# Kernel tuning notes

Measured on AMD Instinct MI355X. Metric: run time of the kernel, lower is better.

## Reference

```python
import jax, jax.numpy as jnp
import numpy as np

B, N = 64, 1500
F_MIN, F_MAX = 0.5, 3.0  # HR band in Hz (30-180 bpm)
SAMPLING_F = 0.002       # frequency grid step -> F = 1251 frequencies
FS = 30.0                # video frame rate


def setup_inputs() -> dict:
    key = jax.random.key(0)
    k1, k2 = jax.random.split(key)
    x = jax.random.normal(k1, (B, N), dtype=jnp.float32)
    # true frequencies inside the searched band
    f_true = jax.random.uniform(k2, (B,), dtype=jnp.float32, minval=F_MIN, maxval=F_MAX)
    fs = jnp.full((B,), FS, dtype=jnp.float32)
    deltas = jnp.zeros((B,), dtype=jnp.float32)  # accepted but unused by the loss
    return {
        "x": x,
        "f_true": f_true,
        "fs": fs,
        "deltas": deltas,
        "sampling_f": SAMPLING_F,
        "f_range": (F_MIN, F_MAX),
    }


def reference(x, f_true, fs, deltas, sampling_f, f_range):
    f_min, f_max = f_range
    # frequency grid, same semantics as torch.arange(f_min, f_max+step, step)
    f_values = jnp.arange(f_min, f_max + sampling_f, sampling_f, dtype=jnp.float32)  # [F]
    n = jnp.arange(x.shape[1], dtype=jnp.float32)  # [N] time indices
    # angles[b,f,n] = 2*pi * f_values[f] * n / fs[b]  (fs varies per sample)
    phase = (2.0 * jnp.pi) * (f_values[None, :, None] * n[None, None, :]) / fs[:, None, None]  # [B,F,N]
    # PSD at each grid frequency: (sum x cos)^2 + (sum x sin)^2, batched as one contraction
    cos_terms = jnp.einsum('bn,bfn->bf', x, jnp.cos(phase))  # [B,F]
    sin_terms = jnp.einsum('bn,bfn->bf', x, jnp.sin(phase))  # [B,F]
    psd = cos_terms ** 2 + sin_terms ** 2                    # [B,F]
    log_lik = jnp.log(jax.nn.softmax(psd, axis=1) + 1e-8)    # [B,F]
    # index of grid frequency closest to f_true (non-differentiable gather index)
    idx = jnp.argmin(jnp.abs(f_values[None, :] - f_true[:, None]), axis=1)  # [B]
    per_sample = -jnp.take_along_axis(log_lik, idx[:, None], axis=1)[:, 0]  # [B]
    return jnp.mean(per_sample)
```

## Files before the change

kernel.cpp:

```cpp
#include <hip/hip_runtime.h>

#define BATCH 64
#define NSAMP 1500
#define NFREQ 1251
#define NSEG  5
#define SEGLEN 300
#define FBLK  256
#define FCHUNKS 5

__global__ __launch_bounds__(256) void goertzel_kernel(
    const float* __restrict__ x,
    const float* __restrict__ fs,
    const float* __restrict__ sampling_f,
    const float* __restrict__ f_range,
    float2* __restrict__ pcs,
    float* __restrict__ out)
{
    __shared__ float4 xs4[SEGLEN / 4];
    const int b   = blockIdx.x;
    const int seg = blockIdx.z;
    const int tid = threadIdx.x;
    const int n0  = seg * SEGLEN;

    if (b == 0 && seg == 0 && blockIdx.y == 0 && tid == 0) out[0] = 0.0f;

    const float4* xg = reinterpret_cast<const float4*>(x + b * NSAMP + n0);
    for (int i = tid; i < SEGLEN / 4; i += FBLK) xs4[i] = xg[i];
    __syncthreads();

    const int fidx = blockIdx.y * FBLK + tid;
    if (fidx >= NFREQ) return;

    const float f_min = f_range[0];
    const float step  = sampling_f[0];
    const float delta = (f_min + step) - f_min;
    const float fv    = f_min + (float)fidx * delta;

    const float rho = fv / fs[b];
    float rf = rho - floorf(rho);
    const float coef = 2.0f * __builtin_amdgcn_cosf(rf);

    float s1 = 0.0f, s2 = 0.0f;
#pragma unroll 5
    for (int k = 0; k < SEGLEN / 4; ++k) {
        float4 v = xs4[k];
        float t;
        t = fmaf(coef, s1, v.x - s2); s2 = s1; s1 = t;
        t = fmaf(coef, s1, v.y - s2); s2 = s1; s1 = t;
        t = fmaf(coef, s1, v.z - s2); s2 = s1; s1 = t;
        t = fmaf(coef, s1, v.w - s2); s2 = s1; s1 = t;
    }

    float aM  = (float)SEGLEN * rho;        aM  -= floorf(aM);
    float aM1 = (float)(SEGLEN - 1) * rho;  aM1 -= floorf(aM1);
    float a0  = (float)n0 * rho;            a0  -= floorf(a0);
    const float cM  = __builtin_amdgcn_cosf(aM);
    const float sM  = __builtin_amdgcn_sinf(aM);
    const float cM1 = __builtin_amdgcn_cosf(aM1);
    const float sM1 = __builtin_amdgcn_sinf(aM1);
    const float c0  = __builtin_amdgcn_cosf(a0);
    const float s0  = __builtin_amdgcn_sinf(a0);

    const float Cl = cM1 * s1 - cM * s2;
    const float Sl = sM1 * s1 - sM * s2;
    const float C  = c0 * Cl - s0 * Sl;
    const float S  = s0 * Cl + c0 * Sl;

    pcs[(b * NSEG + seg) * NFREQ + fidx] = make_float2(C, S);
}

__global__ __launch_bounds__(256) void loss_kernel(
    const float2* __restrict__ pcs,
    const float* __restrict__ f_true,
    const float* __restrict__ sampling_f,
    const float* __restrict__ f_range,
    float* __restrict__ out)
{
    const int b   = blockIdx.x;
    const int tid = threadIdx.x;

    __shared__ float psd_s[NFREQ];
    __shared__ float smax[256];
    __shared__ float ssum[256];
    __shared__ float sdist[256];
    __shared__ int   sidx[256];

    const float f_min = f_range[0];
    const float step  = sampling_f[0];
    const float delta = (f_min + step) - f_min;
    const float ft    = f_true[b];

    float vmax  = -INFINITY;
    float bestd = INFINITY;
    int   besti = NFREQ;
    for (int i = tid; i < NFREQ; i += 256) {
        float c = 0.0f, s = 0.0f;
#pragma unroll
        for (int g = 0; g < NSEG; ++g) {
            float2 v = pcs[(b * NSEG + g) * NFREQ + i];
            c += v.x; s += v.y;
        }
        float v = fmaf(c, c, s * s);
        psd_s[i] = v;
        vmax = fmaxf(vmax, v);
        float fv = f_min + (float)i * delta;
        float d  = fabsf(fv - ft);
        if (d < bestd) { bestd = d; besti = i; }
    }
    smax[tid] = vmax; sdist[tid] = bestd; sidx[tid] = besti;
    __syncthreads();
    for (int s = 128; s > 0; s >>= 1) {
        if (tid < s) {
            smax[tid] = fmaxf(smax[tid], smax[tid + s]);
            float d2 = sdist[tid + s]; int i2 = sidx[tid + s];
            if (d2 < sdist[tid] || (d2 == sdist[tid] && i2 < sidx[tid])) {
                sdist[tid] = d2; sidx[tid] = i2;
            }
        }
        __syncthreads();
    }
    const float gmax = smax[0];
    const int   idx  = sidx[0];

    float se = 0.0f;
    for (int i = tid; i < NFREQ; i += 256) se += __expf(psd_s[i] - gmax);
    ssum[tid] = se;
    __syncthreads();
    for (int s = 128; s > 0; s >>= 1) {
        if (tid < s) ssum[tid] += ssum[tid + s];
        __syncthreads();
    }

    if (tid == 0) {
        float sm = __expf(psd_s[idx] - gmax) / ssum[0];
        float per = -logf(sm + 1e-8f);
        atomicAdd(out, per * (1.0f / (float)BATCH));
    }
}

extern "C" void kernel_launch(void* const* d_in, const int* in_sizes, int n_in,
                              void* d_out, int out_size, void* d_ws, size_t ws_size,
                              hipStream_t stream) {
    const float* x          = (const float*)d_in[0];
    const float* f_true     = (const float*)d_in[1];
    const float* fs         = (const float*)d_in[2];
    const float* sampling_f = (const float*)d_in[4];
    const float* f_range    = (const float*)d_in[5];

    float2* pcs = (float2*)d_ws;

    dim3 g1(BATCH, FCHUNKS, NSEG);
    goertzel_kernel<<<g1, FBLK, 0, stream>>>(x, fs, sampling_f, f_range, pcs,
                                             (float*)d_out);
    loss_kernel<<<BATCH, 256, 0, stream>>>(pcs, f_true, sampling_f, f_range,
                                           (float*)d_out);
}
```

Baseline: 76.88 us.

## Fuse Goertzel and loss kernels using last-block-done atomic counters

Merges the two kernels into one launch. An atomic counter per batch row lets the last finishing block of that row compute the softmax loss, and a second global counter lets the last row block reduce the per-sample losses deterministically, replacing the float atomicAdd. This removes one kernel launch and the gap between launches, but adds a memset launch to reset the counters, threadfences, and a larger shared-memory footprint for every block, which may lower occupancy.

```diff
diff --git a/kernel.cpp b/kernel.cpp
--- a/kernel.cpp
+++ b/kernel.cpp
@@ -7,29 +7,43 @@
 #define SEGLEN 300
 #define FBLK  256
 #define FCHUNKS 5
+#define BLOCKS_PER_B (FCHUNKS * NSEG)
 
-__global__ __launch_bounds__(256) void goertzel_kernel(
+#define PCS_ELEMS   (BATCH * NSEG * NFREQ)
+#define PER_OFF     (PCS_ELEMS * 8)
+#define CNT_OFF     (PER_OFF + 256)
+#define CNT2_OFF    (CNT_OFF + 256)
+
+__global__ __launch_bounds__(256) void fused_kernel(
     const float* __restrict__ x,
     const float* __restrict__ fs,
+    const float* __restrict__ f_true,
     const float* __restrict__ sampling_f,
     const float* __restrict__ f_range,
     float2* __restrict__ pcs,
+    float* __restrict__ per_sample,
+    unsigned* __restrict__ cnt,
+    unsigned* __restrict__ cnt2,
     float* __restrict__ out)
 {
     __shared__ float4 xs4[SEGLEN / 4];
+    __shared__ float  psd_s[NFREQ];
+    __shared__ float  smax[256];
+    __shared__ float  ssum[256];
+    __shared__ float  sdist[256];
+    __shared__ int    sidx[256];
+    __shared__ unsigned tick;
+
     const int b   = blockIdx.x;
     const int seg = blockIdx.z;
     const int tid = threadIdx.x;
     const int n0  = seg * SEGLEN;
-
-    if (b == 0 && seg == 0 && blockIdx.y == 0 && tid == 0) out[0] = 0.0f;
 
     const float4* xg = reinterpret_cast<const float4*>(x + b * NSAMP + n0);
     for (int i = tid; i < SEGLEN / 4; i += FBLK) xs4[i] = xg[i];
     __syncthreads();
 
     const int fidx = blockIdx.y * FBLK + tid;
-    if (fidx >= NFREQ) return;
 
     const float f_min = f_range[0];
     const float step  = sampling_f[0];
@@ -66,30 +80,16 @@
     const float C  = c0 * Cl - s0 * Sl;
     const float S  = s0 * Cl + c0 * Sl;
 
-    pcs[(b * NSEG + seg) * NFREQ + fidx] = make_float2(C, S);
-}
+    if (fidx < NFREQ)
+        pcs[(b * NSEG + seg) * NFREQ + fidx] = make_float2(C, S);
 
-__global__ __launch_bounds__(256) void loss_kernel(
-    const float2* __restrict__ pcs,
-    const float* __restrict__ f_true,
-    const float* __restrict__ sampling_f,
-    const float* __restrict__ f_range,
-    float* __restrict__ out)
-{
-    const int b   = blockIdx.x;
-    const int tid = threadIdx.x;
+    __threadfence();
+    if (tid == 0) tick = atomicAdd(&cnt[b], 1u);
+    __syncthreads();
+    if (tick != BLOCKS_PER_B - 1) return;
+    __threadfence();
 
-    __shared__ float psd_s[NFREQ];
-    __shared__ float smax[256];
-    __shared__ float ssum[256];
-    __shared__ float sdist[256];
-    __shared__ int   sidx[256];
-
-    const float f_min = f_range[0];
-    const float step  = sampling_f[0];
-    const float delta = (f_min + step) - f_min;
-    const float ft    = f_true[b];
-
+    const float ft = f_true[b];
     float vmax  = -INFINITY;
     float bestd = INFINITY;
     int   besti = NFREQ;
@@ -103,8 +103,8 @@
         float v = fmaf(c, c, s * s);
         psd_s[i] = v;
         vmax = fmaxf(vmax, v);
-        float fv = f_min + (float)i * delta;
-        float d  = fabsf(fv - ft);
+        float fg = f_min + (float)i * delta;
+        float d  = fabsf(fg - ft);
         if (d < bestd) { bestd = d; besti = i; }
     }
     smax[tid] = vmax; sdist[tid] = bestd; sidx[tid] = besti;
@@ -133,8 +133,19 @@
 
     if (tid == 0) {
         float sm = __expf(psd_s[idx] - gmax) / ssum[0];
-        float per = -logf(sm + 1e-8f);
-        atomicAdd(out, per * (1.0f / (float)BATCH));
+        per_sample[b] = -logf(sm + 1e-8f);
+    }
+
+    __threadfence();
+    if (tid == 0) tick = atomicAdd(cnt2, 1u);
+    __syncthreads();
+    if (tick != BATCH - 1) return;
+    __threadfence();
+
+    if (tid < 64) {
+        float v = per_sample[tid];
+        for (int off = 32; off > 0; off >>= 1) v += __shfl_down(v, off);
+        if (tid == 0) out[0] = v * (1.0f / (float)BATCH);
     }
 }
 
@@ -147,11 +158,16 @@
     const float* sampling_f = (const float*)d_in[4];
     const float* f_range    = (const float*)d_in[5];
 
-    float2* pcs = (float2*)d_ws;
+    char* ws = (char*)d_ws;
+    float2*   pcs        = (float2*)ws;
+    float*    per_sample = (float*)(ws + PER_OFF);
+    unsigned* cnt        = (unsigned*)(ws + CNT_OFF);
+    unsigned* cnt2       = (unsigned*)(ws + CNT2_OFF);
 
-    dim3 g1(BATCH, FCHUNKS, NSEG);
-    goertzel_kernel<<<g1, FBLK, 0, stream>>>(x, fs, sampling_f, f_range, pcs,
-                                             (float*)d_out);
-    loss_kernel<<<BATCH, 256, 0, stream>>>(pcs, f_true, sampling_f, f_range,
-                                           (float*)d_out);
+    hipMemsetAsync(ws + CNT_OFF, 0, 512, stream);
+
+    dim3 g(BATCH, FCHUNKS, NSEG);
+    fused_kernel<<<g, FBLK, 0, stream>>>(x, fs, f_true, sampling_f, f_range,
+                                         pcs, per_sample, cnt, cnt2,
+                                         (float*)d_out);
 }
```

Result: slower. 194.8 us (+153.4%).

## Run all five Goertzel segments per thread and write PSD directly

Applied to the files above, without the earlier changes.

Each block now loads the whole signal and every thread runs five independent Goertzel recurrences, one per segment, interleaved for ILP. The segments are combined in registers, so the kernel writes a single PSD value instead of five partial complex sums. This shortens the serial dependency chain and removes the 5x workspace traffic plus the summation in the loss kernel. The loss kernel's tree reductions are also replaced with wavefront shuffle reductions. In exchange the grid shrinks from 1600 to 320 blocks, which may leave the GPU underoccupied, and register use per thread rises.

```diff
diff --git a/kernel.cpp b/kernel.cpp
--- a/kernel.cpp
+++ b/kernel.cpp
@@ -13,23 +13,20 @@
     const float* __restrict__ fs,
     const float* __restrict__ sampling_f,
     const float* __restrict__ f_range,
-    float2* __restrict__ pcs,
+    float* __restrict__ psd,
     float* __restrict__ out)
 {
-    __shared__ float4 xs4[SEGLEN / 4];
+    __shared__ float4 xs4[NSAMP / 4];
     const int b   = blockIdx.x;
-    const int seg = blockIdx.z;
     const int tid = threadIdx.x;
-    const int n0  = seg * SEGLEN;
 
-    if (b == 0 && seg == 0 && blockIdx.y == 0 && tid == 0) out[0] = 0.0f;
+    if (b == 0 && blockIdx.y == 0 && tid == 0) out[0] = 0.0f;
 
-    const float4* xg = reinterpret_cast<const float4*>(x + b * NSAMP + n0);
-    for (int i = tid; i < SEGLEN / 4; i += FBLK) xs4[i] = xg[i];
+    const float4* xg = reinterpret_cast<const float4*>(x + b * NSAMP);
+    for (int i = tid; i < NSAMP / 4; i += FBLK) xs4[i] = xg[i];
     __syncthreads();
 
     const int fidx = blockIdx.y * FBLK + tid;
-    if (fidx >= NFREQ) return;
 
     const float f_min = f_range[0];
     const float step  = sampling_f[0];
@@ -40,99 +37,116 @@
     float rf = rho - floorf(rho);
     const float coef = 2.0f * __builtin_amdgcn_cosf(rf);
 
-    float s1 = 0.0f, s2 = 0.0f;
-#pragma unroll 5
+    float s1[NSEG], s2[NSEG];
+#pragma unroll
+    for (int g = 0; g < NSEG; ++g) { s1[g] = 0.0f; s2[g] = 0.0f; }
+
+#pragma unroll 3
     for (int k = 0; k < SEGLEN / 4; ++k) {
-        float4 v = xs4[k];
-        float t;
-        t = fmaf(coef, s1, v.x - s2); s2 = s1; s1 = t;
-        t = fmaf(coef, s1, v.y - s2); s2 = s1; s1 = t;
-        t = fmaf(coef, s1, v.z - s2); s2 = s1; s1 = t;
-        t = fmaf(coef, s1, v.w - s2); s2 = s1; s1 = t;
+#pragma unroll
+        for (int g = 0; g < NSEG; ++g) {
+            float4 v = xs4[g * (SEGLEN / 4) + k];
+            float t;
+            t = fmaf(coef, s1[g], v.x - s2[g]); s2[g] = s1[g]; s1[g] = t;
+            t = fmaf(coef, s1[g], v.y - s2[g]); s2[g] = s1[g]; s1[g] = t;
+            t = fmaf(coef, s1[g], v.z - s2[g]); s2[g] = s1[g]; s1[g] = t;
+            t = fmaf(coef, s1[g], v.w - s2[g]); s2[g] = s1[g]; s1[g] = t;
+        }
     }
 
     float aM  = (float)SEGLEN * rho;        aM  -= floorf(aM);
     float aM1 = (float)(SEGLEN - 1) * rho;  aM1 -= floorf(aM1);
-    float a0  = (float)n0 * rho;            a0  -= floorf(a0);
     const float cM  = __builtin_amdgcn_cosf(aM);
     const float sM  = __builtin_amdgcn_sinf(aM);
     const float cM1 = __builtin_amdgcn_cosf(aM1);
     const float sM1 = __builtin_amdgcn_sinf(aM1);
-    const float c0  = __builtin_amdgcn_cosf(a0);
-    const float s0  = __builtin_amdgcn_sinf(a0);
 
-    const float Cl = cM1 * s1 - cM * s2;
-    const float Sl = sM1 * s1 - sM * s2;
-    const float C  = c0 * Cl - s0 * Sl;
-    const float S  = s0 * Cl + c0 * Sl;
+    float C = 0.0f, S = 0.0f;
+#pragma unroll
+    for (int g = 0; g < NSEG; ++g) {
+        float a0 = (float)(g * SEGLEN) * rho;  a0 -= floorf(a0);
+        const float c0 = __builtin_amdgcn_cosf(a0);
+        const float s0 = __builtin_amdgcn_sinf(a0);
+        const float Cl = cM1 * s1[g] - cM * s2[g];
+        const float Sl = sM1 * s1[g] - sM * s2[g];
+        C += c0 * Cl - s0 * Sl;
+        S += s0 * Cl + c0 * Sl;
+    }
 
-    pcs[(b * NSEG + seg) * NFREQ + fidx] = make_float2(C, S);
+    if (fidx < NFREQ)
+        psd[b * NFREQ + fidx] = fmaf(C, C, S * S);
 }
 
 __global__ __launch_bounds__(256) void loss_kernel(
-    const float2* __restrict__ pcs,
+    const float* __restrict__ psd,
     const float* __restrict__ f_true,
     const float* __restrict__ sampling_f,
     const float* __restrict__ f_range,
     float* __restrict__ out)
 {
-    const int b   = blockIdx.x;
-    const int tid = threadIdx.x;
+    const int b    = blockIdx.x;
+    const int tid  = threadIdx.x;
+    const int wave = tid >> 6;
+    const int lane = tid & 63;
 
     __shared__ float psd_s[NFREQ];
-    __shared__ float smax[256];
-    __shared__ float ssum[256];
-    __shared__ float sdist[256];
-    __shared__ int   sidx[256];
+    __shared__ float wmax[4];
+    __shared__ float wdist[4];
+    __shared__ int   widx[4];
+    __shared__ float wsum[4];
+    __shared__ float s_gmax;
+    __shared__ int   s_idx;
 
     const float f_min = f_range[0];
     const float step  = sampling_f[0];
     const float delta = (f_min + step) - f_min;
     const float ft    = f_true[b];
+    const float* p    = psd + b * NFREQ;
 
     float vmax  = -INFINITY;
     float bestd = INFINITY;
     int   besti = NFREQ;
     for (int i = tid; i < NFREQ; i += 256) {
-        float c = 0.0f, s = 0.0f;
-#pragma unroll
-        for (int g = 0; g < NSEG; ++g) {
-            float2 v = pcs[(b * NSEG + g) * NFREQ + i];
-            c += v.x; s += v.y;
-        }
-        float v = fmaf(c, c, s * s);
+        float v = p[i];
         psd_s[i] = v;
         vmax = fmaxf(vmax, v);
-        float fv = f_min + (float)i * delta;
-        float d  = fabsf(fv - ft);
+        float fg = f_min + (float)i * delta;
+        float d  = fabsf(fg - ft);
         if (d < bestd) { bestd = d; besti = i; }
     }
-    smax[tid] = vmax; sdist[tid] = bestd; sidx[tid] = besti;
+    for (int off = 32; off > 0; off >>= 1) {
+        float m2 = __shfl_down(vmax, off);
+        float d2 = __shfl_down(bestd, off);
+        int   i2 = __shfl_down(besti, off);
+        vmax = fmaxf(vmax, m2);
+        if (d2 < bestd || (d2 == bestd && i2 < besti)) { bestd = d2; besti = i2; }
+    }
+    if (lane == 0) { wmax[wave] = vmax; wdist[wave] = bestd; widx[wave] = besti; }
     __syncthreads();
-    for (int s = 128; s > 0; s >>= 1) {
-        if (tid < s) {
-            smax[tid] = fmaxf(smax[tid], smax[tid + s]);
-            float d2 = sdist[tid + s]; int i2 = sidx[tid + s];
-            if (d2 < sdist[tid] || (d2 == sdist[tid] && i2 < sidx[tid])) {
-                sdist[tid] = d2; sidx[tid] = i2;
+    if (tid == 0) {
+        float gm = wmax[0]; float bd = wdist[0]; int bi = widx[0];
+#pragma unroll
+        for (int w = 1; w < 4; ++w) {
+            gm = fmaxf(gm, wmax[w]);
+            if (wdist[w] < bd || (wdist[w] == bd && widx[w] < bi)) {
+                bd = wdist[w]; bi = widx[w];
             }
         }
-        __syncthreads();
+        s_gmax = gm; s_idx = bi;
     }
-    const float gmax = smax[0];
-    const int   idx  = sidx[0];
+    __syncthreads();
+    const float gmax = s_gmax;
+    const int   idx  = s_idx;
 
     float se = 0.0f;
     for (int i = tid; i < NFREQ; i += 256) se += __expf(psd_s[i] - gmax);
-    ssum[tid] = se;
+    for (int off = 32; off > 0; off >>= 1) se += __shfl_down(se, off);
+    if (lane == 0) wsum[wave] = se;
     __syncthreads();
-    for (int s = 128; s > 0; s >>= 1) {
-        if (tid < s) ssum[tid] += ssum[tid + s];
-        __syncthreads();
-    }
 
     if (tid == 0) {
-        float sm = __expf(psd_s[idx] - gmax) / ssum[0];
+        float sumexp = wsum[0] + wsum[1] + wsum[2] + wsum[3];
+        float sm = __expf(psd_s[idx] - gmax) / sumexp;
         float per = -logf(sm + 1e-8f);
         atomicAdd(out, per * (1.0f / (float)BATCH));
     }
@@ -147,11 +161,11 @@
     const float* sampling_f = (const float*)d_in[4];
     const float* f_range    = (const float*)d_in[5];
 
-    float2* pcs = (float2*)d_ws;
+    float* psd = (float*)d_ws;
 
-    dim3 g1(BATCH, FCHUNKS, NSEG);
-    goertzel_kernel<<<g1, FBLK, 0, stream>>>(x, fs, sampling_f, f_range, pcs,
+    dim3 g1(BATCH, FCHUNKS);
+    goertzel_kernel<<<g1, FBLK, 0, stream>>>(x, fs, sampling_f, f_range, psd,
                                              (float*)d_out);
-    loss_kernel<<<BATCH, 256, 0, stream>>>(pcs, f_true, sampling_f, f_range,
+    loss_kernel<<<BATCH, 256, 0, stream>>>(psd, f_true, sampling_f, f_range,
                                            (float*)d_out);
 }
```

Result: slower. 81.38 us (+5.9%).
